# Optimization experiments

Measured on AMD Instinct MI355X. Metric: run time of the kernel, lower is better.

Reference implementation:

```python
import jax, jax.numpy as jnp
import numpy as np

C = 40.0
DIM_H = 50  # feature dim is 2*DIM_H = 100


def setup_inputs() -> dict:
    key = jax.random.key(0)
    k1, k2, k3, k4 = jax.random.split(key, 4)
    B, L, H = 512, 512, 2 * DIM_H
    data = jax.random.normal(k1, (B, L, H), dtype=jnp.float32)
    aspect_Index = jax.random.randint(k2, (B,), 0, 100, dtype=jnp.int64)
    aspect_len = jax.random.randint(k3, (B,), 0, 10, dtype=jnp.int64)
    sents_len = jax.random.randint(k4, (B,), 0, 512, dtype=jnp.int64)
    return {"data": data, "aspect_Index": aspect_Index,
            "aspect_len": aspect_len, "sents_len": sents_len}


def reference(data, aspect_Index, aspect_len, sents_len):
    # data: [B, L, H]. Position-decay mask, broadcast over H.
    B, L, H = data.shape
    i = jnp.arange(L)[None, :]                      # [1, L] position index
    i_f = i.astype(data.dtype)
    a_end = (aspect_Index + aspect_len)[:, None]    # [B, 1] aspect end (exclusive)
    a_end_f = a_end.astype(data.dtype)
    a_idx_f = aspect_Index[:, None].astype(data.dtype)
    s_len = sents_len[:, None]                      # [B, 1]
    # i < a_end        -> 1 - (a_end - i)/C
    # a_end <= i < len -> 1 - (i - a_idx)/C
    # else             -> 0
    mask = jnp.where(i < a_end, 1.0 - (a_end_f - i_f) / C,
                     jnp.where(i < s_len, 1.0 - (i_f - a_idx_f) / C, 0.0))
    return data * mask[:, :, None]
```

## Files before the change

### kernel.cpp

```cpp
#include <hip/hip_runtime.h>


constexpr int kL = 512;
constexpr int kH = 100;
constexpr float kInvC = 1.0f / 40.0f;

typedef float f32x4 __attribute__((ext_vector_type(4)));

__global__ __launch_bounds__(256) void mask_mul_kernel(
    const f32x4* __restrict__ data,
    const int* __restrict__ a_idx,
    const int* __restrict__ a_len,
    const int* __restrict__ s_len,
    f32x4* __restrict__ out)
{
    const int idx = blockIdx.x * blockDim.x + threadIdx.x;
    const int e   = idx * 4;
    const int bl = e / kH;
    const int l  = bl & (kL - 1);
    const int b  = bl >> 9;

    const int aI = a_idx[b];
    const int aE = aI + a_len[b];
    const int sL = s_len[b];

    float m;
    if (l < aE)       m = 1.0f - (float)(aE - l) * kInvC;
    else if (l < sL)  m = 1.0f - (float)(l - aI) * kInvC;
    else              m = 0.0f;

    f32x4 v = __builtin_nontemporal_load(&data[idx]);
    v *= m;
    __builtin_nontemporal_store(v, &out[idx]);
}

extern "C" void kernel_launch(void* const* d_in, const int* in_sizes, int n_in,
                              void* d_out, int out_size, void* d_ws, size_t ws_size,
                              hipStream_t stream) {
    const float* data = (const float*)d_in[0];
    const int* a_idx  = (const int*)d_in[1];
    const int* a_len  = (const int*)d_in[2];
    const int* s_len  = (const int*)d_in[3];
    float* out        = (float*)d_out;

    const int n4 = out_size / 4;
    const int threads = 256;
    const int blocks = (n4 + threads - 1) / threads;

    mask_mul_kernel<<<blocks, threads, 0, stream>>>(
        (const f32x4*)data, a_idx, a_len, s_len, (f32x4*)out);
}
```

Measured before the change: 180.1 us.

## Skip loading data for masked-out rows and process half-batch per block

Each block now handles half of one batch's rows in a strided loop, so the per-batch parameters are loaded once per block. The loop no longer divides per element to find the batch. Rows at or beyond max(aspect end, sentence length) get zero mask, so their input loads are skipped and zeros are written directly, which removes roughly half of the read traffic for random lengths. The cost is a much smaller grid (1024 blocks) with loops, which may lower memory-level parallelism.

```diff
diff --git a/kernel.cpp b/kernel.cpp
--- a/kernel.cpp
+++ b/kernel.cpp
@@ -1,37 +1,49 @@
 #include <hip/hip_runtime.h>
 
 
-constexpr int kL = 512;
-constexpr int kH = 100;
-constexpr float kInvC = 1.0f / 40.0f;
+constexpr int kL        = 512;
+constexpr int kF4PerRow = 25;
+constexpr int kF4PerB   = kL * kF4PerRow;
+constexpr int kChunkF4  = kF4PerB / 2;
+constexpr float kInvC   = 1.0f / 40.0f;
 
 typedef float f32x4 __attribute__((ext_vector_type(4)));
 
-__global__ __launch_bounds__(256) void mask_mul_kernel(
+__global__ __launch_bounds__(256, 4) void mask_mul_kernel(
     const f32x4* __restrict__ data,
     const int* __restrict__ a_idx,
     const int* __restrict__ a_len,
     const int* __restrict__ s_len,
     f32x4* __restrict__ out)
 {
-    const int idx = blockIdx.x * blockDim.x + threadIdx.x;
-    const int e   = idx * 4;
-    const int bl = e / kH;
-    const int l  = bl & (kL - 1);
-    const int b  = bl >> 9;
+    const int b     = blockIdx.x >> 1;
+    const int chunk = blockIdx.x & 1;
 
     const int aI = a_idx[b];
     const int aE = aI + a_len[b];
     const int sL = s_len[b];
+    const int zs = max(aE, sL);
 
-    float m;
-    if (l < aE)       m = 1.0f - (float)(aE - l) * kInvC;
-    else if (l < sL)  m = 1.0f - (float)(l - aI) * kInvC;
-    else              m = 0.0f;
+    const int base4 = b * kF4PerB + chunk * kChunkF4;
+    const int l0    = chunk * (kL / 2);
 
-    f32x4 v = __builtin_nontemporal_load(&data[idx]);
-    v *= m;
-    __builtin_nontemporal_store(v, &out[idx]);
+    #pragma unroll 5
+    for (int i = threadIdx.x; i < kChunkF4; i += 256) {
+        const int idx4 = base4 + i;
+        const int l    = l0 + (int)((unsigned)i / 25u);
+
+        float m;
+        if (l < aE)       m = 1.0f - (float)(aE - l) * kInvC;
+        else if (l < sL)  m = 1.0f - (float)(l - aI) * kInvC;
+        else              m = 0.0f;
+
+        f32x4 v = {0.0f, 0.0f, 0.0f, 0.0f};
+        if (l < zs) {
+            v = __builtin_nontemporal_load(&data[idx4]);
+            v *= m;
+        }
+        __builtin_nontemporal_store(v, &out[idx4]);
+    }
 }
 
 extern "C" void kernel_launch(void* const* d_in, const int* in_sizes, int n_in,
@@ -43,9 +55,9 @@
     const int* s_len  = (const int*)d_in[3];
     float* out        = (float*)d_out;
 
-    const int n4 = out_size / 4;
+    const int B = out_size / (kL * 100);
+    const int blocks = B * 2;
     const int threads = 256;
-    const int blocks = (n4 + threads - 1) / threads;
 
     mask_mul_kernel<<<blocks, threads, 0, stream>>>(
         (const f32x4*)data, a_idx, a_len, s_len, (f32x4*)out);
```

Measured after the change: 179.2 us (median of 2 runs). About the same (-0.5%).
